# Kernel tuning notes

Measured on AMD Instinct MI355X. Metric: run time of the kernel, lower is better.

## Reference

```python
import jax, jax.numpy as jnp
import numpy as np

D = 64       # embed_dim
K = 1024     # n_embed
B, T = 16, 4096


def setup_inputs() -> dict:
    key = jax.random.key(0)
    k1, k2 = jax.random.split(key)
    inp = jax.random.normal(k1, (B, T, D), dtype=jnp.float32)
    embed = jax.random.normal(k2, (D, K), dtype=jnp.float32)  # codebook buffer, [dim, n_embed]
    return {"input": inp, "embed": embed}


def reference(input, embed):
    # Flatten to [N, D]
    Bv, Tv, Dv = input.shape
    flat = input.reshape(-1, Dv)
    dist = (jnp.sum(flat * flat, axis=1, keepdims=True)
            - 2.0 * (flat @ embed)
            + jnp.sum(embed * embed, axis=0, keepdims=True))
    embed_ind = jnp.argmin(dist, axis=1).reshape(Bv, Tv)       # nearest code per token
    quantize = jnp.take(embed.T, embed_ind, axis=0)            # [B, T, D] codebook gather
    diff = jnp.square(jax.lax.stop_gradient(quantize) - input) # commitment term (elementwise)
    quantize = input + jax.lax.stop_gradient(quantize - input) # straight-through estimator
    return quantize, diff, embed_ind
```

## Files before the change

kernel.cpp:

```cpp
#include <hip/hip_runtime.h>

#define DD 64
#define KK 1024
#define NN 65536

typedef __attribute__((ext_vector_type(8))) short short8v;
typedef __attribute__((ext_vector_type(4))) float f32x4;


__device__ __forceinline__ unsigned short bf16_rn_bits(float f) {
    unsigned u = __builtin_bit_cast(unsigned, f);
    u += 0x7fffu + ((u >> 16) & 1u);
    return (unsigned short)(u >> 16);
}
__device__ __forceinline__ float bf16_bits_to_f(unsigned short h) {
    return __builtin_bit_cast(float, (unsigned)h << 16);
}

__global__ __launch_bounds__(256) void vq_prep(const float* __restrict__ embed,
                                               float* __restrict__ eT,
                                               unsigned short* __restrict__ ehp,
                                               unsigned short* __restrict__ elp,
                                               float* __restrict__ enorm) {
    __shared__ float part[4][64];
    int t  = threadIdx.x;
    int kl = t & 63;
    int dq = t >> 6;
    int k  = blockIdx.x * 64 + kl;
    int tile = k >> 4, r = k & 15;
    float s = 0.f;
#pragma unroll
    for (int i = 0; i < 16; ++i) {
        int d = dq * 16 + i;
        float v = embed[d * KK + k];
        eT[(size_t)k * DD + d] = v;
        unsigned short h = bf16_rn_bits(v);
        float lo = v - bf16_bits_to_f(h);
        int dh = d >> 5, g = (d & 31) >> 3, j = d & 7;
        size_t idx = ((size_t)((tile * 2 + dh) * 64 + g * 16 + r)) * 8 + j;
        ehp[idx] = h;
        elp[idx] = bf16_rn_bits(lo);
        s = fmaf(v, v, s);
    }
    part[dq][kl] = s;
    __syncthreads();
    if (dq == 0) enorm[k] = part[0][kl] + part[1][kl] + part[2][kl] + part[3][kl];
}

__global__ __launch_bounds__(256) void vq_mfma(const float* __restrict__ inp,
                                               const unsigned short* __restrict__ ehp,
                                               const unsigned short* __restrict__ elp,
                                               const float* __restrict__ eT,
                                               const float* __restrict__ enorm,
                                               float* __restrict__ outQ,
                                               float* __restrict__ outDiff,
                                               float* __restrict__ outInd,
                                               unsigned char* __restrict__ flags) {
    __shared__ float s_b1[64][2];
    __shared__ float s_b2[64][2];
    __shared__ int   s_k1[64][2];
    __shared__ int   s_kwin[64];

    int tid  = threadIdx.x;
    int wave = tid >> 6, lane = tid & 63;
    int g = lane >> 4, r = lane & 15;
    int mg = wave >> 1, kh = wave & 1;
    int tokBlk = blockIdx.x * 64;
    int tok0   = tokBlk + mg * 32;

    short8v a_hi[2][2], a_lo[2][2];
#pragma unroll
    for (int m = 0; m < 2; ++m) {
        const float* xrow = inp + (size_t)(tok0 + 16 * m + r) * DD + 8 * g;
#pragma unroll
        for (int dh = 0; dh < 2; ++dh) {
            float4 v0 = *(const float4*)(xrow + 32 * dh);
            float4 v1 = *(const float4*)(xrow + 32 * dh + 4);
            float xv[8] = {v0.x, v0.y, v0.z, v0.w, v1.x, v1.y, v1.z, v1.w};
#pragma unroll
            for (int j = 0; j < 8; ++j) {
                unsigned short h = bf16_rn_bits(xv[j]);
                float lo = xv[j] - bf16_bits_to_f(h);
                a_hi[m][dh][j] = (short)h;
                a_lo[m][dh][j] = (short)bf16_rn_bits(lo);
            }
        }
    }

    float best1[2][4], best2[2][4];
    int k1[2][4];
#pragma unroll
    for (int m = 0; m < 2; ++m)
#pragma unroll
        for (int j = 0; j < 4; ++j) { best1[m][j] = 3.4e38f; best2[m][j] = 3.4e38f; k1[m][j] = 0; }

    const short8v* hp = (const short8v*)ehp;
    const short8v* lp = (const short8v*)elp;

#pragma unroll 2
    for (int t = 0; t < KK / 32; ++t) {
        int tg = kh * 32 + t;
        int c  = tg * 16 + r;
        short8v bhi0 = hp[(tg * 2 + 0) * 64 + lane];
        short8v bhi1 = hp[(tg * 2 + 1) * 64 + lane];
        short8v blo0 = lp[(tg * 2 + 0) * 64 + lane];
        short8v blo1 = lp[(tg * 2 + 1) * 64 + lane];
        float en = enorm[c];

        f32x4 accA0 = {0.f,0.f,0.f,0.f}, accA1 = {0.f,0.f,0.f,0.f};
        f32x4 accB0 = {0.f,0.f,0.f,0.f}, accB1 = {0.f,0.f,0.f,0.f};
        accA0 = __builtin_amdgcn_mfma_f32_16x16x32_bf16(a_hi[0][0], bhi0, accA0, 0, 0, 0);
        accA1 = __builtin_amdgcn_mfma_f32_16x16x32_bf16(a_hi[1][0], bhi0, accA1, 0, 0, 0);
        accB0 = __builtin_amdgcn_mfma_f32_16x16x32_bf16(a_lo[0][0], bhi0, accB0, 0, 0, 0);
        accB1 = __builtin_amdgcn_mfma_f32_16x16x32_bf16(a_lo[1][0], bhi0, accB1, 0, 0, 0);
        accA0 = __builtin_amdgcn_mfma_f32_16x16x32_bf16(a_hi[0][1], bhi1, accA0, 0, 0, 0);
        accA1 = __builtin_amdgcn_mfma_f32_16x16x32_bf16(a_hi[1][1], bhi1, accA1, 0, 0, 0);
        accB0 = __builtin_amdgcn_mfma_f32_16x16x32_bf16(a_lo[0][1], bhi1, accB0, 0, 0, 0);
        accB1 = __builtin_amdgcn_mfma_f32_16x16x32_bf16(a_lo[1][1], bhi1, accB1, 0, 0, 0);
        accA0 = __builtin_amdgcn_mfma_f32_16x16x32_bf16(a_hi[0][0], blo0, accA0, 0, 0, 0);
        accA1 = __builtin_amdgcn_mfma_f32_16x16x32_bf16(a_hi[1][0], blo0, accA1, 0, 0, 0);
        accA0 = __builtin_amdgcn_mfma_f32_16x16x32_bf16(a_hi[0][1], blo1, accA0, 0, 0, 0);
        accA1 = __builtin_amdgcn_mfma_f32_16x16x32_bf16(a_hi[1][1], blo1, accA1, 0, 0, 0);

#pragma unroll
        for (int m = 0; m < 2; ++m) {
            const f32x4& aA = m ? accA1 : accA0;
            const f32x4& aB = m ? accB1 : accB0;
#pragma unroll
            for (int j = 0; j < 4; ++j) {
                float dist = fmaf(-2.f, aA[j] + aB[j], en);
                bool lt1 = dist < best1[m][j];
                bool lt2 = dist < best2[m][j];
                float nb2 = lt1 ? best1[m][j] : (lt2 ? dist : best2[m][j]);
                best1[m][j] = lt1 ? dist : best1[m][j];
                k1[m][j]    = lt1 ? c    : k1[m][j];
                best2[m][j] = nb2;
            }
        }
    }

#pragma unroll
    for (int msk = 1; msk < 16; msk <<= 1) {
#pragma unroll
        for (int m = 0; m < 2; ++m)
#pragma unroll
            for (int j = 0; j < 4; ++j) {
                float ob1 = __shfl_xor(best1[m][j], msk, 64);
                float ob2 = __shfl_xor(best2[m][j], msk, 64);
                int   ok  = __shfl_xor(k1[m][j],   msk, 64);
                bool takeOther = (ob1 < best1[m][j]) || (ob1 == best1[m][j] && ok < k1[m][j]);
                float lose = takeOther ? best1[m][j] : ob1;
                best1[m][j] = takeOther ? ob1 : best1[m][j];
                k1[m][j]    = takeOther ? ok  : k1[m][j];
                best2[m][j] = fminf(fminf(best2[m][j], ob2), lose);
            }
    }

    if (r == 0) {
#pragma unroll
        for (int m = 0; m < 2; ++m)
#pragma unroll
            for (int j = 0; j < 4; ++j) {
                int tl = mg * 32 + m * 16 + 4 * g + j;
                s_b1[tl][kh] = best1[m][j];
                s_b2[tl][kh] = best2[m][j];
                s_k1[tl][kh] = k1[m][j];
            }
    }
    __syncthreads();

    if (tid < 64) {
        float b1a = s_b1[tid][0], b2a = s_b2[tid][0];
        float b1b = s_b1[tid][1], b2b = s_b2[tid][1];
        int   ka  = s_k1[tid][0], kb  = s_k1[tid][1];
        float nb1, nb2; int nk;
        if (b1b < b1a) { nb1 = b1b; nk = kb; nb2 = fminf(b1a, b2b); }
        else           { nb1 = b1a; nk = ka; nb2 = fminf(b2a, b1b); }
        int tok = tokBlk + tid;
        outInd[tok]  = (float)nk;
        flags[tok]   = (nb2 - nb1 < 0.02f) ? 1 : 0;
        s_kwin[tid]  = nk;
    }
    __syncthreads();

#pragma unroll
    for (int tt = 0; tt < 16; ++tt) {
        int tl = wave * 16 + tt;
        int k  = s_kwin[tl];
        float ev = eT[(size_t)k * DD + lane];
        float xv = inp[(size_t)(tokBlk + tl) * DD + lane];
        float d  = ev - xv;
        outQ[(size_t)(tokBlk + tl) * DD + lane]    = ev;
        outDiff[(size_t)(tokBlk + tl) * DD + lane] = d * d;
    }
}

__global__ __launch_bounds__(256) void vq_fixup(const float* __restrict__ inp,
                                                const float* __restrict__ eT,
                                                const unsigned char* __restrict__ flags,
                                                float* __restrict__ outQ,
                                                float* __restrict__ outDiff,
                                                float* __restrict__ outInd) {
    int waveId = blockIdx.x * 4 + (threadIdx.x >> 6);
    int lane   = threadIdx.x & 63;

    for (int iter = 0; iter < NN / 4096; ++iter) {
        int n = waveId + iter * 4096;
        if (!flags[n]) continue;

        float x[DD];
        const float4* xp = (const float4*)(inp + (size_t)n * DD);
#pragma unroll
        for (int i = 0; i < DD / 4; ++i) {
            float4 v = xp[i];
            x[4 * i + 0] = v.x; x[4 * i + 1] = v.y;
            x[4 * i + 2] = v.z; x[4 * i + 3] = v.w;
        }

        double bestd = 1e300;
        int bk = 0;
        for (int c = 0; c < KK / 64; ++c) {
            int k = c * 64 + lane;
            const float4* e4 = (const float4*)(eT + (size_t)k * DD);
            double acc = 0.0;
#pragma unroll
            for (int i = 0; i < DD / 4; ++i) {
                float4 ev = e4[i];
                double dx;
                dx = (double)x[4 * i + 0] - (double)ev.x; acc = fma(dx, dx, acc);
                dx = (double)x[4 * i + 1] - (double)ev.y; acc = fma(dx, dx, acc);
                dx = (double)x[4 * i + 2] - (double)ev.z; acc = fma(dx, dx, acc);
                dx = (double)x[4 * i + 3] - (double)ev.w; acc = fma(dx, dx, acc);
            }
            if (acc < bestd) { bestd = acc; bk = k; }
        }
        for (int off = 32; off > 0; off >>= 1) {
            double od = __shfl_xor(bestd, off);
            int    ok = __shfl_xor(bk, off);
            if (od < bestd || (od == bestd && ok < bk)) { bestd = od; bk = ok; }
        }
        float q  = eT[(size_t)bk * DD + lane];
        float xv = inp[(size_t)n * DD + lane];
        float dd = q - xv;
        outQ[(size_t)n * DD + lane]    = q;
        outDiff[(size_t)n * DD + lane] = dd * dd;
        if (lane == 0) outInd[n] = (float)bk;
    }
}

extern "C" void kernel_launch(void* const* d_in, const int* in_sizes, int n_in,
                              void* d_out, int out_size, void* d_ws, size_t ws_size,
                              hipStream_t stream) {
    const float* inp   = (const float*)d_in[0];
    const float* embed = (const float*)d_in[1];
    float* outQ    = (float*)d_out;
    float* outDiff = outQ + (size_t)NN * DD;
    float* outInd  = outDiff + (size_t)NN * DD;

    char* ws = (char*)d_ws;
    float*          eT    = (float*)(ws);
    unsigned short* ehp   = (unsigned short*)(ws + 262144);
    unsigned short* elp   = (unsigned short*)(ws + 393216);
    float*          enorm = (float*)(ws + 524288);
    unsigned char*  flags = (unsigned char*)(ws + 528384);

    vq_prep <<<16,   256, 0, stream>>>(embed, eT, ehp, elp, enorm);
    vq_mfma <<<1024, 256, 0, stream>>>(inp, ehp, elp, eT, enorm, outQ, outDiff, outInd, flags);
    vq_fixup<<<1024, 256, 0, stream>>>(inp, eT, flags, outQ, outDiff, outInd);
}
```

Baseline: 156.7 us.

## Compact ambiguous tokens into an atomic worklist for the fixup kernel

```diff
diff --git a/kernel.cpp b/kernel.cpp
--- a/kernel.cpp
+++ b/kernel.cpp
@@ -3,6 +3,7 @@
 #define DD 64
 #define KK 1024
 #define NN 65536
+#define FCAP 16384
 
 typedef __attribute__((ext_vector_type(8))) short short8v;
 typedef __attribute__((ext_vector_type(4))) float f32x4;
@@ -21,7 +22,9 @@
                                                float* __restrict__ eT,
                                                unsigned short* __restrict__ ehp,
                                                unsigned short* __restrict__ elp,
-                                               float* __restrict__ enorm) {
+                                               float* __restrict__ enorm,
+                                               int* __restrict__ fcount) {
+    if (blockIdx.x == 0 && threadIdx.x == 0) *fcount = 0;
     __shared__ float part[4][64];
     int t  = threadIdx.x;
     int kl = t & 63;
@@ -55,7 +58,8 @@
                                                float* __restrict__ outQ,
                                                float* __restrict__ outDiff,
                                                float* __restrict__ outInd,
-                                               unsigned char* __restrict__ flags) {
+                                               int* __restrict__ fcount,
+                                               int* __restrict__ flist) {
     __shared__ float s_b1[64][2];
     __shared__ float s_b2[64][2];
     __shared__ int   s_k1[64][2];
@@ -178,8 +182,11 @@
         else           { nb1 = b1a; nk = ka; nb2 = fminf(b2a, b1b); }
         int tok = tokBlk + tid;
         outInd[tok]  = (float)nk;
-        flags[tok]   = (nb2 - nb1 < 0.02f) ? 1 : 0;
         s_kwin[tid]  = nk;
+        if (nb2 - nb1 < 0.02f) {
+            int idx = atomicAdd(fcount, 1);
+            if (idx < FCAP) flist[idx] = tok;
+        }
     }
     __syncthreads();
 
@@ -196,42 +203,46 @@
 }
 
 __global__ __launch_bounds__(256) void vq_fixup(const float* __restrict__ inp,
+                                                const float* __restrict__ embed,
                                                 const float* __restrict__ eT,
-                                                const unsigned char* __restrict__ flags,
+                                                const int* __restrict__ fcount,
+                                                const int* __restrict__ flist,
                                                 float* __restrict__ outQ,
                                                 float* __restrict__ outDiff,
                                                 float* __restrict__ outInd) {
-    int waveId = blockIdx.x * 4 + (threadIdx.x >> 6);
-    int lane   = threadIdx.x & 63;
-
-    for (int iter = 0; iter < NN / 4096; ++iter) {
-        int n = waveId + iter * 4096;
-        if (!flags[n]) continue;
+    int wid  = blockIdx.x * 4 + (threadIdx.x >> 6);
+    int lane = threadIdx.x & 63;
+    int nt   = *fcount;
+    if (nt > FCAP) nt = FCAP;
+
+    for (int i = wid; i < nt; i += 1024) {
+        int n = flist[i];
 
         float x[DD];
         const float4* xp = (const float4*)(inp + (size_t)n * DD);
 #pragma unroll
-        for (int i = 0; i < DD / 4; ++i) {
-            float4 v = xp[i];
-            x[4 * i + 0] = v.x; x[4 * i + 1] = v.y;
-            x[4 * i + 2] = v.z; x[4 * i + 3] = v.w;
+        for (int q = 0; q < DD / 4; ++q) {
+            float4 v = xp[q];
+            x[4 * q + 0] = v.x; x[4 * q + 1] = v.y;
+            x[4 * q + 2] = v.z; x[4 * q + 3] = v.w;
         }
 
         double bestd = 1e300;
         int bk = 0;
         for (int c = 0; c < KK / 64; ++c) {
             int k = c * 64 + lane;
-            const float4* e4 = (const float4*)(eT + (size_t)k * DD);
-            double acc = 0.0;
-#pragma unroll
-            for (int i = 0; i < DD / 4; ++i) {
-                float4 ev = e4[i];
-                double dx;
-                dx = (double)x[4 * i + 0] - (double)ev.x; acc = fma(dx, dx, acc);
-                dx = (double)x[4 * i + 1] - (double)ev.y; acc = fma(dx, dx, acc);
-                dx = (double)x[4 * i + 2] - (double)ev.z; acc = fma(dx, dx, acc);
-                dx = (double)x[4 * i + 3] - (double)ev.w; acc = fma(dx, dx, acc);
-            }
+            const float* ecol = embed + k;
+            double acc0 = 0.0, acc1 = 0.0;
+#pragma unroll
+            for (int d = 0; d < DD; d += 2) {
+                float e0 = ecol[(size_t)d * KK];
+                float e1 = ecol[(size_t)(d + 1) * KK];
+                double dx0 = (double)x[d]     - (double)e0;
+                double dx1 = (double)x[d + 1] - (double)e1;
+                acc0 = fma(dx0, dx0, acc0);
+                acc1 = fma(dx1, dx1, acc1);
+            }
+            double acc = acc0 + acc1;
             if (acc < bestd) { bestd = acc; bk = k; }
         }
         for (int off = 32; off > 0; off >>= 1) {
@@ -258,13 +269,14 @@
     float* outInd  = outDiff + (size_t)NN * DD;
 
     char* ws = (char*)d_ws;
-    float*          eT    = (float*)(ws);
-    unsigned short* ehp   = (unsigned short*)(ws + 262144);
-    unsigned short* elp   = (unsigned short*)(ws + 393216);
-    float*          enorm = (float*)(ws + 524288);
-    unsigned char*  flags = (unsigned char*)(ws + 528384);
-
-    vq_prep <<<16,   256, 0, stream>>>(embed, eT, ehp, elp, enorm);
-    vq_mfma <<<1024, 256, 0, stream>>>(inp, ehp, elp, eT, enorm, outQ, outDiff, outInd, flags);
-    vq_fixup<<<1024, 256, 0, stream>>>(inp, eT, flags, outQ, outDiff, outInd);
-}
+    float*          eT     = (float*)(ws);
+    unsigned short* ehp    = (unsigned short*)(ws + 262144);
+    unsigned short* elp    = (unsigned short*)(ws + 393216);
+    float*          enorm  = (float*)(ws + 524288);
+    int*            fcount = (int*)(ws + 528384);
+    int*            flist  = (int*)(ws + 528400);
+
+    vq_prep <<<16,   256, 0, stream>>>(embed, eT, ehp, elp, enorm, fcount);
+    vq_mfma <<<1024, 256, 0, stream>>>(inp, ehp, elp, eT, enorm, outQ, outDiff, outInd, fcount, flist);
+    vq_fixup<<<256,  256, 0, stream>>>(inp, embed, eT, fcount, flist, outQ, outDiff, outInd);
+}
```

After: 129.4 us. -17.4%, faster.
